# Optimization experiments

Hardware: AMD Instinct MI355X
Metric: run time of the kernel (lower is better)

## Reference

```python
import jax, jax.numpy as jnp
import numpy as np

N_HEAD = 16
WINDOW = 128
CAUSAL = False


def setup_inputs() -> dict:
    key = jax.random.key(0)
    ks = jax.random.split(key, 5)
    B, T, D = 1, 4096, 1024
    x = jax.random.normal(ks[0], (B, T, D), dtype=jnp.float32)
    w_in = jax.random.normal(ks[1], (3 * D, D), dtype=jnp.float32) * 0.02
    b_in = jax.random.normal(ks[2], (3 * D,), dtype=jnp.float32) * 0.02
    w_out = jax.random.normal(ks[3], (D, D), dtype=jnp.float32) * 0.02
    b_out = jax.random.normal(ks[4], (D,), dtype=jnp.float32) * 0.02
    return {"x": x, "w_in": w_in, "b_in": b_in, "w_out": w_out, "b_out": b_out}


def _window_attention(x, w_in, b_in, w_out, b_out):
    B, T, D = x.shape
    H = N_HEAD
    hd = D // H
    scale = 1.0 / jnp.sqrt(jnp.float32(hd))

    # fused in-projection, as in torch nn.MultiheadAttention (y = x @ W^T + b)
    qkv = jnp.einsum('btd,ed->bte', x, w_in) + b_in  # (B, T, 3D)
    q, k, v = jnp.split(qkv, 3, axis=-1)
    # (B, H, T, hd)
    q = q.reshape(B, T, H, hd).transpose(0, 2, 1, 3)
    k = k.reshape(B, T, H, hd).transpose(0, 2, 1, 3)
    v = v.reshape(B, T, H, hd).transpose(0, 2, 1, 3)

    scores = jnp.einsum('bhqd,bhkd->bhqk', q, k) * scale  # (B, H, T, T)

    idx = jnp.arange(T)
    diff = idx[:, None] - idx[None, :]
    if CAUSAL:
        allowed = (diff >= 0) & (diff <= WINDOW)
    else:
        allowed = jnp.abs(diff) <= WINDOW
    NEG = jnp.float32(-1e30)
    scores = jnp.where(allowed[None, None, :, :], scores, NEG)

    attn = jax.nn.softmax(scores, axis=-1)
    ctx = jnp.einsum('bhqk,bhkd->bhqd', attn, v)  # (B, H, T, hd)
    ctx = ctx.transpose(0, 2, 1, 3).reshape(B, T, D)
    out = jnp.einsum('btd,ed->bte', ctx, w_out) + b_out
    return x + out  # residual, as in the module


def reference(x, w_in, b_in, w_out, b_out):
    return _window_attention(x, w_in, b_in, w_out, b_out)
```

## Files before the change

kernel.cpp:

```cpp
#include <hip/hip_runtime.h>

#define T_SEQ 4096
#define DMODEL 1024
#define NHEAD 16
#define HDIM 64
#define WIN 128

typedef __attribute__((ext_vector_type(8))) short bf16x8;
typedef __attribute__((ext_vector_type(4))) float f32x4;
typedef __attribute__((ext_vector_type(4))) unsigned short u16x4;

__device__ __forceinline__ unsigned short f2bf(float f) {
  unsigned int u = __builtin_bit_cast(unsigned int, f);
  return (unsigned short)((u + 0x7fffu + ((u >> 16) & 1u)) >> 16);
}

__device__ __forceinline__ void gload_lds16(const unsigned short* g,
                                            unsigned short* l) {
  __builtin_amdgcn_global_load_lds(
      (const __attribute__((address_space(1))) void*)g,
      (__attribute__((address_space(3))) void*)l, 16, 0, 0);
}

__global__ void convert_all(const float* __restrict__ x,
                            const float* __restrict__ w_in,
                            const float* __restrict__ w_out,
                            unsigned short* __restrict__ x_bf,
                            unsigned short* __restrict__ w_in_bf,
                            unsigned short* __restrict__ w_out_bf) {
  int stride = gridDim.x * blockDim.x;
  int t0 = blockIdx.x * blockDim.x + threadIdx.x;
#define CVT(SRC, DST, N4)                                          \
  for (int i = t0; i < (N4); i += stride) {                        \
    float4 v = reinterpret_cast<const float4*>(SRC)[i];            \
    u16x4 o;                                                       \
    o.x = f2bf(v.x); o.y = f2bf(v.y); o.z = f2bf(v.z); o.w = f2bf(v.w); \
    reinterpret_cast<u16x4*>(DST)[i] = o;                          \
  }
  CVT(x, x_bf, T_SEQ * DMODEL / 4)
  CVT(w_in, w_in_bf, 3 * DMODEL * DMODEL / 4)
  CVT(w_out, w_out_bf, DMODEL * DMODEL / 4)
#undef CVT
}

template <int EPI, int BM, int BN>
__device__ __forceinline__ void gemm_body(
    const unsigned short* __restrict__ A,
    const unsigned short* __restrict__ B,
    const float* __restrict__ bias,
    unsigned short* __restrict__ q_buf,
    unsigned short* __restrict__ k_buf,
    unsigned short* __restrict__ vt_buf,
    const float* __restrict__ x_res,
    float* __restrict__ out) {
  const int K = DMODEL;
  constexpr int NT = DMODEL / 64;
  constexpr int SM = BM / 2, SN = BN / 2;
  constexpr int MR = SM / 16, NR = SN / 16;
  constexpr int AL = BM / 32, BL = BN / 32;
  __shared__ __align__(16) unsigned short As[2 * BM * 64];
  __shared__ __align__(16) unsigned short Bs[2 * BN * 64];

  int tid = threadIdx.x;
  int lane = tid & 63, wave = tid >> 6;
  int wr = wave >> 1, wc = wave & 1;
  int lo = lane & 15, hi = lane >> 4;
  int t0 = blockIdx.y * BM, e0 = blockIdx.x * BN;

  f32x4 acc[MR][NR];
#pragma unroll
  for (int m = 0; m < MR; ++m)
#pragma unroll
    for (int n = 0; n < NR; ++n) acc[m][n] = (f32x4){0.f, 0.f, 0.f, 0.f};

  int c8 = (tid & 7) ^ ((tid >> 3) & 7);
  int srow = tid >> 3;
  const unsigned short* AbaseG = A + (size_t)(t0 + srow) * K + c8 * 8;
  const unsigned short* BbaseG = B + (size_t)(e0 + srow) * K + c8 * 8;
  unsigned short* ldsAu = As + wave * 512;
  unsigned short* ldsBu = Bs + wave * 512;

  auto stage = [&](int tt) {
    int k0 = tt * 64;
    int ab = (tt & 1) * (BM * 64);
    int bb = (tt & 1) * (BN * 64);
#pragma unroll
    for (int l = 0; l < AL; ++l)
      gload_lds16(AbaseG + (size_t)l * 32 * K + k0, ldsAu + l * 2048 + ab);
#pragma unroll
    for (int l = 0; l < BL; ++l)
      gload_lds16(BbaseG + (size_t)l * 32 * K + k0, ldsBu + l * 2048 + bb);
  };

  stage(0);
  asm volatile("s_waitcnt vmcnt(0) lgkmcnt(0)\n\ts_barrier" ::: "memory");

  for (int t = 0; t < NT; ++t) {
    if (t + 1 < NT) stage(t + 1);
    const unsigned short* Ab = As + (t & 1) * (BM * 64);
    const unsigned short* Bb = Bs + (t & 1) * (BN * 64);
    bf16x8 af[MR][2], bfr[NR][2];
#pragma unroll
    for (int m = 0; m < MR; ++m) {
      int row = wr * SM + m * 16 + lo;
#pragma unroll
      for (int ks = 0; ks < 2; ++ks)
        af[m][ks] = *reinterpret_cast<const bf16x8*>(
            &Ab[row * 64 + (((ks << 2) + hi) ^ (row & 7)) * 8]);
    }
#pragma unroll
    for (int n = 0; n < NR; ++n) {
      int row = wc * SN + n * 16 + lo;
#pragma unroll
      for (int ks = 0; ks < 2; ++ks)
        bfr[n][ks] = *reinterpret_cast<const bf16x8*>(
            &Bb[row * 64 + (((ks << 2) + hi) ^ (row & 7)) * 8]);
    }
#pragma unroll
    for (int ks = 0; ks < 2; ++ks)
#pragma unroll
      for (int m = 0; m < MR; ++m)
#pragma unroll
        for (int n = 0; n < NR; ++n)
          acc[m][n] = __builtin_amdgcn_mfma_f32_16x16x32_bf16(af[m][ks], bfr[n][ks],
                                                              acc[m][n], 0, 0, 0);
    asm volatile("s_waitcnt vmcnt(0) lgkmcnt(0)\n\ts_barrier" ::: "memory");
  }

  int t0w = t0 + wr * SM;
  int e0w = e0 + wc * SN;
#pragma unroll
  for (int m = 0; m < MR; ++m) {
#pragma unroll
    for (int n = 0; n < NR; ++n) {
      int e = e0w + n * 16 + lo;
      float bv = bias[e];
      if (EPI == 0) {
        int part = e >> 10;
        int h = (e >> 6) & 15;
        int d = e & 63;
        if (part == 2) {
          int t = t0w + m * 16 + hi * 4;
          u16x4 pk;
          pk.x = f2bf(acc[m][n][0] + bv);
          pk.y = f2bf(acc[m][n][1] + bv);
          pk.z = f2bf(acc[m][n][2] + bv);
          pk.w = f2bf(acc[m][n][3] + bv);
          *reinterpret_cast<u16x4*>(&vt_buf[((size_t)(h * HDIM + d)) * T_SEQ + t]) = pk;
        } else {
          unsigned short* dst = (part == 0) ? q_buf : k_buf;
#pragma unroll
          for (int jj = 0; jj < 4; ++jj) {
            int t = t0w + m * 16 + hi * 4 + jj;
            dst[((size_t)h * T_SEQ + t) * HDIM + d] = f2bf(acc[m][n][jj] + bv);
          }
        }
      } else {
#pragma unroll
        for (int jj = 0; jj < 4; ++jj) {
          int t = t0w + m * 16 + hi * 4 + jj;
          size_t idxo = (size_t)t * DMODEL + e;
          out[idxo] = acc[m][n][jj] + bv + x_res[idxo];
        }
      }
    }
  }
}

__global__ __launch_bounds__(256) void qkv_gemm(
    const unsigned short* __restrict__ A, const unsigned short* __restrict__ B,
    const float* __restrict__ bias, unsigned short* __restrict__ q_buf,
    unsigned short* __restrict__ k_buf, unsigned short* __restrict__ vt_buf) {
  gemm_body<0, 128, 192>(A, B, bias, q_buf, k_buf, vt_buf, nullptr, nullptr);
}

__global__ __launch_bounds__(256) void out_gemm(
    const unsigned short* __restrict__ A, const unsigned short* __restrict__ B,
    const float* __restrict__ bias, const float* __restrict__ x_res,
    float* __restrict__ out) {
  gemm_body<1, 128, 64>(A, B, bias, nullptr, nullptr, nullptr, x_res, out);
}

__global__ __launch_bounds__(256) void win_attn(
    const unsigned short* __restrict__ q_buf,
    const unsigned short* __restrict__ k_buf,
    const unsigned short* __restrict__ vt_buf,
    unsigned short* __restrict__ ctx) {
  __shared__ __align__(16) unsigned short p_lds[4][2][16 * 40];
  int tid = threadIdx.x;
  int wave = tid >> 6;
  int lane = tid & 63;
  int lo = lane & 15, hi = lane >> 4;

  int id = blockIdx.x;
  int sw = (id & 7) * (512 / 8) + (id >> 3);
  int job = sw * 4 + wave;
  int h = job >> 7;
  int q0 = (job & 127) * 32;
  const float SC = 0.18033688011112042f;

  bf16x8 aq[2][2];
#pragma unroll
  for (int u = 0; u < 2; ++u) {
    const unsigned short* qrow =
        q_buf + ((size_t)h * T_SEQ + q0 + u * 16 + lo) * HDIM + hi * 8;
    aq[u][0] = *reinterpret_cast<const bf16x8*>(qrow);
    aq[u][1] = *reinterpret_cast<const bf16x8*>(qrow + 32);
  }

  float L[2][4] = {{0.f, 0.f, 0.f, 0.f}, {0.f, 0.f, 0.f, 0.f}};
  f32x4 o[2][4];
#pragma unroll
  for (int u = 0; u < 2; ++u)
#pragma unroll
    for (int n = 0; n < 4; ++n) o[u][n] = (f32x4){0.f, 0.f, 0.f, 0.f};

  int jstart = q0 - WIN; if (jstart < 0) jstart = 0;
  int jend = q0 + 32 + WIN; if (jend > T_SEQ) jend = T_SEQ;

  bf16x8 kc[2][2], vc[4];
#pragma unroll
  for (int c = 0; c < 2; ++c) {
    const unsigned short* kp =
        k_buf + ((size_t)h * T_SEQ + jstart + c * 16 + lo) * HDIM + hi * 8;
    kc[c][0] = *reinterpret_cast<const bf16x8*>(kp);
    kc[c][1] = *reinterpret_cast<const bf16x8*>(kp + 32);
  }
#pragma unroll
  for (int n = 0; n < 4; ++n)
    vc[n] = *reinterpret_cast<const bf16x8*>(
        vt_buf + ((size_t)(h * HDIM + n * 16 + lo)) * T_SEQ + jstart + hi * 8);

  for (int j0 = jstart; j0 < jend; j0 += 32) {
    int jn = (j0 + 32 < jend) ? j0 + 32 : jstart;
    bf16x8 kn[2][2], vn[4];
#pragma unroll
    for (int c = 0; c < 2; ++c) {
      const unsigned short* kp =
          k_buf + ((size_t)h * T_SEQ + jn + c * 16 + lo) * HDIM + hi * 8;
      kn[c][0] = *reinterpret_cast<const bf16x8*>(kp);
      kn[c][1] = *reinterpret_cast<const bf16x8*>(kp + 32);
    }
#pragma unroll
    for (int n = 0; n < 4; ++n)
      vn[n] = *reinterpret_cast<const bf16x8*>(
          vt_buf + ((size_t)(h * HDIM + n * 16 + lo)) * T_SEQ + jn + hi * 8);
#pragma unroll
    for (int u = 0; u < 2; ++u) {
#pragma unroll
      for (int c = 0; c < 2; ++c) {
        f32x4 z = (f32x4){0.f, 0.f, 0.f, 0.f};
        __builtin_amdgcn_s_setprio(1);
        z = __builtin_amdgcn_mfma_f32_16x16x32_bf16(aq[u][0], kc[c][0], z, 0, 0, 0);
        z = __builtin_amdgcn_mfma_f32_16x16x32_bf16(aq[u][1], kc[c][1], z, 0, 0, 0);
        __builtin_amdgcn_s_setprio(0);
        int kj = j0 + c * 16 + lo;
#pragma unroll
        for (int jq = 0; jq < 4; ++jq) {
          int q = q0 + u * 16 + hi * 4 + jq;
          bool ok = (q - kj <= WIN) && (kj - q <= WIN);
          float p = ok ? __builtin_amdgcn_exp2f(z[jq] * SC) : 0.f;
          L[u][jq] += p;
          p_lds[wave][u][(hi * 4 + jq) * 40 + c * 16 + lo] = f2bf(p);
        }
      }
    }
    bf16x8 pa[2];
    pa[0] = *reinterpret_cast<const bf16x8*>(&p_lds[wave][0][lo * 40 + hi * 8]);
    pa[1] = *reinterpret_cast<const bf16x8*>(&p_lds[wave][1][lo * 40 + hi * 8]);
    __builtin_amdgcn_s_setprio(1);
#pragma unroll
    for (int n = 0; n < 4; ++n) {
      o[0][n] = __builtin_amdgcn_mfma_f32_16x16x32_bf16(pa[0], vc[n], o[0][n], 0, 0, 0);
      o[1][n] = __builtin_amdgcn_mfma_f32_16x16x32_bf16(pa[1], vc[n], o[1][n], 0, 0, 0);
    }
    __builtin_amdgcn_s_setprio(0);
#pragma unroll
    for (int c = 0; c < 2; ++c) {
      kc[c][0] = kn[c][0];
      kc[c][1] = kn[c][1];
    }
#pragma unroll
    for (int n = 0; n < 4; ++n) vc[n] = vn[n];
  }
#pragma unroll
  for (int u = 0; u < 2; ++u)
#pragma unroll
    for (int jq = 0; jq < 4; ++jq) {
#pragma unroll
      for (int w = 1; w < 16; w <<= 1) L[u][jq] += __shfl_xor(L[u][jq], w, 64);
    }
#pragma unroll
  for (int u = 0; u < 2; ++u)
#pragma unroll
    for (int jq = 0; jq < 4; ++jq) {
      int t = q0 + u * 16 + hi * 4 + jq;
      float inv = 1.f / L[u][jq];
#pragma unroll
      for (int n = 0; n < 4; ++n)
        ctx[(size_t)t * DMODEL + h * HDIM + n * 16 + lo] = f2bf(o[u][n][jq] * inv);
    }
}

extern "C" void kernel_launch(void* const* d_in, const int* in_sizes, int n_in,
                              void* d_out, int out_size, void* d_ws, size_t ws_size,
                              hipStream_t stream) {
  const float* x = (const float*)d_in[0];
  const float* w_in = (const float*)d_in[1];
  const float* b_in = (const float*)d_in[2];
  const float* w_out = (const float*)d_in[3];
  const float* b_out = (const float*)d_in[4];
  float* out = (float*)d_out;

  char* ws = (char*)d_ws;
  size_t off = 0;
  auto take = [&](size_t bytes) {
    char* p = ws + off;
    off += (bytes + 255) & ~(size_t)255;
    return p;
  };
  unsigned short* x_bf = (unsigned short*)take((size_t)T_SEQ * DMODEL * 2);
  unsigned short* w_in_bf = (unsigned short*)take((size_t)3 * DMODEL * DMODEL * 2);
  unsigned short* w_out_bf = (unsigned short*)take((size_t)DMODEL * DMODEL * 2);
  unsigned short* q_buf = (unsigned short*)take((size_t)T_SEQ * DMODEL * 2);
  unsigned short* k_buf = (unsigned short*)take((size_t)T_SEQ * DMODEL * 2);
  unsigned short* vt_buf = (unsigned short*)take((size_t)T_SEQ * DMODEL * 2 + 8192);
  unsigned short* ctx = (unsigned short*)take((size_t)T_SEQ * DMODEL * 2);

  convert_all<<<2048, 256, 0, stream>>>(x, w_in, w_out, x_bf, w_in_bf, w_out_bf);

  dim3 g1(3 * DMODEL / 192, T_SEQ / 128);
  qkv_gemm<<<g1, 256, 0, stream>>>(x_bf, w_in_bf, b_in, q_buf, k_buf, vt_buf);

  win_attn<<<512, 256, 0, stream>>>(q_buf, k_buf, vt_buf, ctx);

  dim3 g2(DMODEL / 64, T_SEQ / 128);
  out_gemm<<<g2, 256, 0, stream>>>(ctx, w_out_bf, b_out, x, out);
}
```

Baseline: 89.84 us.

## Switch GEMM to 4-slot, 3-deep prefetch pipeline with K-step 32

Restructures the GEMM main loop from double-buffered 64-wide K tiles to a 4-slot ring of 32-wide K tiles, keeping three stages in flight with partial vmcnt waits instead of draining all loads each iteration. The LDS swizzle is adapted to 32-element rows, and MFMA blocks are wrapped in s_setprio to favor math issue. This aims to hide global-to-LDS latency better, at the cost of more barriers per K and hand-tuned waitcnt values that must match the per-stage load count.

```diff
diff --git a/kernel.cpp b/kernel.cpp
--- a/kernel.cpp
+++ b/kernel.cpp
@@ -54,12 +54,14 @@
     const float* __restrict__ x_res,
     float* __restrict__ out) {
   const int K = DMODEL;
-  constexpr int NT = DMODEL / 64;
+  constexpr int NS = DMODEL / 32;
   constexpr int SM = BM / 2, SN = BN / 2;
   constexpr int MR = SM / 16, NR = SN / 16;
-  constexpr int AL = BM / 32, BL = BN / 32;
-  __shared__ __align__(16) unsigned short As[2 * BM * 64];
-  __shared__ __align__(16) unsigned short Bs[2 * BN * 64];
+  constexpr int AL = BM / 64, BL = BN / 64;
+  constexpr int SI = AL + BL;
+  constexpr int SLOT_A = BM * 32, SLOT_B = BN * 32;
+  __shared__ __align__(16) unsigned short As[4 * SLOT_A];
+  __shared__ __align__(16) unsigned short Bs[4 * SLOT_B];
 
   int tid = threadIdx.x;
   int lane = tid & 63, wave = tid >> 6;
@@ -73,59 +75,67 @@
 #pragma unroll
     for (int n = 0; n < NR; ++n) acc[m][n] = (f32x4){0.f, 0.f, 0.f, 0.f};
 
-  int c8 = (tid & 7) ^ ((tid >> 3) & 7);
-  int srow = tid >> 3;
-  const unsigned short* AbaseG = A + (size_t)(t0 + srow) * K + c8 * 8;
-  const unsigned short* BbaseG = B + (size_t)(e0 + srow) * K + c8 * 8;
-  unsigned short* ldsAu = As + wave * 512;
-  unsigned short* ldsBu = Bs + wave * 512;
-
-  auto stage = [&](int tt) {
-    int k0 = tt * 64;
-    int ab = (tt & 1) * (BM * 64);
-    int bb = (tt & 1) * (BN * 64);
+  int srow = tid >> 2;
+  int cswz = (tid & 3) ^ ((tid >> 3) & 3);
+  const unsigned short* AG = A + (size_t)(t0 + srow) * K + cswz * 8;
+  const unsigned short* BG = B + (size_t)(e0 + srow) * K + cswz * 8;
+  unsigned short* ldsA = As + wave * 512;
+  unsigned short* ldsB = Bs + wave * 512;
+
+  auto stage = [&](int s) {
+    int k0 = s * 32;
+    int sl = s & 3;
 #pragma unroll
     for (int l = 0; l < AL; ++l)
-      gload_lds16(AbaseG + (size_t)l * 32 * K + k0, ldsAu + l * 2048 + ab);
+      gload_lds16(AG + (size_t)l * 64 * K + k0, ldsA + sl * SLOT_A + l * 2048);
 #pragma unroll
     for (int l = 0; l < BL; ++l)
-      gload_lds16(BbaseG + (size_t)l * 32 * K + k0, ldsBu + l * 2048 + bb);
+      gload_lds16(BG + (size_t)l * 64 * K + k0, ldsB + sl * SLOT_B + l * 2048);
   };
 
-  stage(0);
-  asm volatile("s_waitcnt vmcnt(0) lgkmcnt(0)\n\ts_barrier" ::: "memory");
-
-  for (int t = 0; t < NT; ++t) {
-    if (t + 1 < NT) stage(t + 1);
-    const unsigned short* Ab = As + (t & 1) * (BM * 64);
-    const unsigned short* Bb = Bs + (t & 1) * (BN * 64);
-    bf16x8 af[MR][2], bfr[NR][2];
+  auto compute = [&](int s) {
+    int sl = s & 3;
+    const unsigned short* Ab = As + sl * SLOT_A;
+    const unsigned short* Bb = Bs + sl * SLOT_B;
+    bf16x8 af[MR], bfr[NR];
 #pragma unroll
     for (int m = 0; m < MR; ++m) {
       int row = wr * SM + m * 16 + lo;
-#pragma unroll
-      for (int ks = 0; ks < 2; ++ks)
-        af[m][ks] = *reinterpret_cast<const bf16x8*>(
-            &Ab[row * 64 + (((ks << 2) + hi) ^ (row & 7)) * 8]);
+      af[m] = *reinterpret_cast<const bf16x8*>(
+          &Ab[row * 32 + (hi ^ ((row >> 1) & 3)) * 8]);
     }
 #pragma unroll
     for (int n = 0; n < NR; ++n) {
       int row = wc * SN + n * 16 + lo;
-#pragma unroll
-      for (int ks = 0; ks < 2; ++ks)
-        bfr[n][ks] = *reinterpret_cast<const bf16x8*>(
-            &Bb[row * 64 + (((ks << 2) + hi) ^ (row & 7)) * 8]);
-    }
-#pragma unroll
-    for (int ks = 0; ks < 2; ++ks)
-#pragma unroll
-      for (int m = 0; m < MR; ++m)
-#pragma unroll
-        for (int n = 0; n < NR; ++n)
-          acc[m][n] = __builtin_amdgcn_mfma_f32_16x16x32_bf16(af[m][ks], bfr[n][ks],
-                                                              acc[m][n], 0, 0, 0);
-    asm volatile("s_waitcnt vmcnt(0) lgkmcnt(0)\n\ts_barrier" ::: "memory");
-  }
+      bfr[n] = *reinterpret_cast<const bf16x8*>(
+          &Bb[row * 32 + (hi ^ ((row >> 1) & 3)) * 8]);
+    }
+    __builtin_amdgcn_s_setprio(1);
+#pragma unroll
+    for (int m = 0; m < MR; ++m)
+#pragma unroll
+      for (int n = 0; n < NR; ++n)
+        acc[m][n] = __builtin_amdgcn_mfma_f32_16x16x32_bf16(af[m], bfr[n],
+                                                            acc[m][n], 0, 0, 0);
+    __builtin_amdgcn_s_setprio(0);
+  };
+
+  stage(0);
+  stage(1);
+  stage(2);
+#define WB(NN) asm volatile("s_waitcnt vmcnt(" #NN ")\n\ts_barrier" ::: "memory")
+  for (int s = 0; s < NS - 3; ++s) {
+    if constexpr (SI == 5) WB(10); else WB(6);
+    stage(s + 3);
+    compute(s);
+  }
+  if constexpr (SI == 5) WB(10); else WB(6);
+  compute(NS - 3);
+  if constexpr (SI == 5) WB(5); else WB(3);
+  compute(NS - 2);
+  WB(0);
+  compute(NS - 1);
+#undef WB
 
   int t0w = t0 + wr * SM;
   int e0w = e0 + wc * SN;
```

Result: slower. 95.08 us (+5.8%).
